# Kernel optimization log

Hardware: AMD Instinct MI355X
Metric: run time of the kernel (lower is better)

## Reference

```python
import jax, jax.numpy as jnp
import numpy as np

MODEL_DIM = 512
NUM_HEADS = 16
D_OUTPUT = 128
DIM_PER_HEAD = MODEL_DIM // NUM_HEADS  # 32
LN_EPS = 1e-5


def setup_inputs() -> dict:
    key = jax.random.key(0)
    ks = jax.random.split(key, 12)
    B = 128
    proj = MODEL_DIM * D_OUTPUT  # 65536
    s = 0.02
    return {
        "key": jax.random.normal(ks[0], (B, 1, MODEL_DIM), jnp.float32),
        "value": jax.random.normal(ks[1], (B, 1, MODEL_DIM), jnp.float32),
        "query": jax.random.normal(ks[2], (B, 1, MODEL_DIM), jnp.float32),
        "Wk": jax.random.normal(ks[3], (MODEL_DIM, proj), jnp.float32) * s,
        "bk": jnp.zeros((proj,), jnp.float32),
        "Wv": jax.random.normal(ks[4], (MODEL_DIM, proj), jnp.float32) * s,
        "bv": jnp.zeros((proj,), jnp.float32),
        "Wq": jax.random.normal(ks[5], (MODEL_DIM, proj), jnp.float32) * s,
        "bq": jnp.zeros((proj,), jnp.float32),
        "Wo": jax.random.normal(ks[6], (MODEL_DIM, MODEL_DIM), jnp.float32) * s,
        "bo": jnp.zeros((MODEL_DIM,), jnp.float32),
        "gamma": jnp.ones((MODEL_DIM,), jnp.float32),
        "beta": jnp.zeros((MODEL_DIM,), jnp.float32),
    }


def reference(key, value, query, Wk, bk, Wv, bv, Wq, bq, Wo, bo, gamma, beta):
    B = key.shape[0]
    residual = query  # [B, 1, model_dim]
    # QKV projections to model_dim*d_output, then view as (B*H, d_output, dim_per_head)
    k = (key @ Wk + bk).reshape(B * NUM_HEADS, -1, DIM_PER_HEAD)
    v = (value @ Wv + bv).reshape(B * NUM_HEADS, -1, DIM_PER_HEAD)
    q = (query @ Wq + bq).reshape(B * NUM_HEADS, -1, DIM_PER_HEAD)
    # faithful to original: scale = (dim_per_head // num_heads) ** -0.5 (int div)
    scale = (DIM_PER_HEAD // NUM_HEADS) ** (-0.5)
    scores = jnp.einsum('bqd,bkd->bqk', q, k) * scale  # [B*H, S, S]
    attn = jax.nn.softmax(scores, axis=2)
    context = jnp.einsum('bqk,bkd->bqd', attn, v)  # [B*H, S, dph]
    context = context.reshape(B, -1, DIM_PER_HEAD * NUM_HEADS)  # [B, d_output, model_dim]
    out = context @ Wo + bo
    x = residual + out  # broadcast [B,1,D] + [B,d_output,D]
    mu = jnp.mean(x, axis=-1, keepdims=True)
    var = jnp.mean(jnp.square(x - mu), axis=-1, keepdims=True)
    out = (x - mu) * jax.lax.rsqrt(var + LN_EPS) * gamma + beta
    return out, attn
```

## Files before the change

### kernel.cpp

```cpp
#include <hip/hip_runtime.h>

typedef unsigned short u16;
typedef unsigned int u32;
typedef __attribute__((ext_vector_type(4))) float f32x4;
typedef __attribute__((ext_vector_type(4))) u16 u16x4;
typedef __attribute__((ext_vector_type(8))) u16 u16x8;
typedef __attribute__((ext_vector_type(8))) __bf16 bf16x8;

#define DEV static __device__ __forceinline__

DEV u16 f2b(float f) {
  u32 u = __builtin_bit_cast(u32, f);
  u32 r = (u + 0x7fffu + ((u >> 16) & 1u)) >> 16;
  return (u16)r;
}

DEV bf16x8 mk8(u16x4 lo, u16x4 hi) {
  u16x8 v = __builtin_shufflevector(lo, hi, 0, 1, 2, 3, 4, 5, 6, 7);
  return __builtin_bit_cast(bf16x8, v);
}

__global__ __launch_bounds__(256) void prep_x(
    const float* __restrict__ key, const float* __restrict__ value,
    const float* __restrict__ query, u16* __restrict__ Xb)
{
  int idx = blockIdx.x * 256 + threadIdx.x;
  int mat = idx >> 14;
  int off = (idx & 16383) * 4;
  const float* src = mat == 0 ? key : (mat == 1 ? value : query);
  f32x4 v = *(const f32x4*)(src + off);
  u16x4 o;
#pragma unroll
  for (int i = 0; i < 4; ++i) o[i] = __builtin_bit_cast(u16, (__bf16)v[i]);
  *(u16x4*)(Xb + mat * 65536 + off) = o;
}

__global__ __launch_bounds__(256, 2) void qkv_gemm(
    const u16* __restrict__ Xb,
    const float* __restrict__ Wk, const float* __restrict__ bk,
    const float* __restrict__ Wv, const float* __restrict__ bv,
    const float* __restrict__ Wq, const float* __restrict__ bq,
    u16* __restrict__ Kp, u16* __restrict__ Vp, u16* __restrict__ Qp)
{
  const int mat = blockIdx.y;
  const float* W    = mat == 0 ? Wk : (mat == 1 ? Wv : Wq);
  const float* bias = mat == 0 ? bk : (mat == 1 ? bv : bq);
  u16* out          = mat == 0 ? Kp : (mat == 1 ? Vp : Qp);
  const u16* Xm = Xb + mat * 65536;
  const int n0 = blockIdx.x * 128;

  const int t = threadIdx.x, lane = t & 63, wid = t >> 6;
  const int wm = wid >> 1, wn = wid & 1;
  const int l15 = lane & 15, lg = lane >> 4;
  const int col0 = n0 + wn * 64 + l15;

  f32x4 acc[4][4];
#pragma unroll
  for (int i = 0; i < 4; ++i)
#pragma unroll
    for (int j = 0; j < 4; ++j) acc[i][j] = (f32x4){0.f, 0.f, 0.f, 0.f};

#pragma unroll 2
  for (int ks = 0; ks < 16; ++ks) {
    const int krow = ks * 32 + lg * 8;
    bf16x8 af[4];
#pragma unroll
    for (int mf = 0; mf < 4; ++mf)
      af[mf] = *(const bf16x8*)(Xm + (wm * 64 + mf * 16 + l15) * 512 + krow);
    float bb[8][4];
#pragma unroll
    for (int j = 0; j < 8; ++j) {
      const float* Wr = W + (size_t)(krow + j) * 65536 + col0;
#pragma unroll
      for (int nf = 0; nf < 4; ++nf) bb[j][nf] = Wr[nf * 16];
    }
    bf16x8 bfr[4];
#pragma unroll
    for (int nf = 0; nf < 4; ++nf) {
      bf16x8 v;
#pragma unroll
      for (int j = 0; j < 8; ++j) v[j] = (__bf16)bb[j][nf];
      bfr[nf] = v;
    }
#pragma unroll
    for (int mf = 0; mf < 4; ++mf)
#pragma unroll
      for (int nf = 0; nf < 4; ++nf)
        acc[mf][nf] = __builtin_amdgcn_mfma_f32_16x16x32_bf16(af[mf], bfr[nf], acc[mf][nf], 0, 0, 0);
  }

#pragma unroll
  for (int nf = 0; nf < 4; ++nf) {
    int col = wn * 64 + nf * 16 + l15;
    float bv_ = bias[n0 + col];
#pragma unroll
    for (int mf = 0; mf < 4; ++mf) {
      int row0 = wm * 64 + mf * 16 + lg * 4;
#pragma unroll
      for (int r = 0; r < 4; ++r) {
        out[(size_t)(row0 + r) * 65536 + n0 + col] = f2b(acc[mf][nf][r] + bv_);
      }
    }
  }
}

__global__ __launch_bounds__(256) void attn_kernel(
    const u16* __restrict__ Qp, const u16* __restrict__ Kp, const u16* __restrict__ Vp,
    float* __restrict__ attnOut, u16* __restrict__ ctx)
{
  const int bh = blockIdx.x;
  const int b = bh >> 4, h = bh & 15;
  const size_t base = (size_t)b * 65536 + h * 4096;

  __shared__ u16 qS[8 * 512];
  __shared__ u16 kS[8 * 512];
  __shared__ u16 vS[32 * 128];
  __shared__ u16 pS[32 * 512];

  const int t = threadIdx.x;
  const int lane = t & 63, w = t >> 6;
  const int l15 = lane & 15, lg = lane >> 4;

#pragma unroll
  for (int p = 0; p < 2; ++p) {
    int idx = p * 256 + t;
    int s = idx >> 2, dc = idx & 3;
    u16x8 qv = *(const u16x8*)(Qp + base + s * 32 + dc * 8);
    u16x8 kv = *(const u16x8*)(Kp + base + s * 32 + dc * 8);
    u16x8 vv = *(const u16x8*)(Vp + base + s * 32 + dc * 8);
    *(u16x4*)(qS + (dc * 2) * 512 + s * 4)     = __builtin_shufflevector(qv, qv, 0, 1, 2, 3);
    *(u16x4*)(qS + (dc * 2 + 1) * 512 + s * 4) = __builtin_shufflevector(qv, qv, 4, 5, 6, 7);
    *(u16x4*)(kS + (dc * 2) * 512 + s * 4)     = __builtin_shufflevector(kv, kv, 0, 1, 2, 3);
    *(u16x4*)(kS + (dc * 2 + 1) * 512 + s * 4) = __builtin_shufflevector(kv, kv, 4, 5, 6, 7);
#pragma unroll
    for (int i = 0; i < 8; ++i)
      vS[(s >> 2) * 128 + (dc * 8 + i) * 4 + (s & 3)] = vv[i];
  }
  __syncthreads();

  f32x4 sc[2][8];
#pragma unroll
  for (int i = 0; i < 2; ++i)
#pragma unroll
    for (int j = 0; j < 8; ++j) sc[i][j] = (f32x4){0.f, 0.f, 0.f, 0.f};

  {
    const int kqA = lg * 2;
    bf16x8 aq[2];
#pragma unroll
    for (int mf = 0; mf < 2; ++mf) {
      int m = w * 32 + mf * 16 + l15;
      u16x4 lo = *(const u16x4*)(qS + kqA * 512 + m * 4);
      u16x4 hi = *(const u16x4*)(qS + (kqA + 1) * 512 + m * 4);
      aq[mf] = mk8(lo, hi);
    }
#pragma unroll
    for (int nf = 0; nf < 8; ++nf) {
      int j = nf * 16 + l15;
      u16x4 lo = *(const u16x4*)(kS + kqA * 512 + j * 4);
      u16x4 hi = *(const u16x4*)(kS + (kqA + 1) * 512 + j * 4);
      bf16x8 bk8 = mk8(lo, hi);
#pragma unroll
      for (int mf = 0; mf < 2; ++mf)
        sc[mf][nf] = __builtin_amdgcn_mfma_f32_16x16x32_bf16(aq[mf], bk8, sc[mf][nf], 0, 0, 0);
    }
  }

  const float SCL = 0.70710678118654752f;
#pragma unroll
  for (int mf = 0; mf < 2; ++mf) {
#pragma unroll
    for (int r = 0; r < 4; ++r) {
      float m8 = -1e30f;
#pragma unroll
      for (int nf = 0; nf < 8; ++nf) m8 = fmaxf(m8, sc[mf][nf][r]);
      m8 = fmaxf(m8, __shfl_xor(m8, 1));
      m8 = fmaxf(m8, __shfl_xor(m8, 2));
      m8 = fmaxf(m8, __shfl_xor(m8, 4));
      m8 = fmaxf(m8, __shfl_xor(m8, 8));
      float s8 = 0.f;
#pragma unroll
      for (int nf = 0; nf < 8; ++nf) {
        float pv = __expf((sc[mf][nf][r] - m8) * SCL);
        sc[mf][nf][r] = pv;
        s8 += pv;
      }
      s8 += __shfl_xor(s8, 1);
      s8 += __shfl_xor(s8, 2);
      s8 += __shfl_xor(s8, 4);
      s8 += __shfl_xor(s8, 8);
      float inv = 1.0f / s8;
      int i = w * 32 + mf * 16 + lg * 4 + r;
      float* ao = attnOut + (size_t)bh * 16384 + (size_t)i * 128;
#pragma unroll
      for (int nf = 0; nf < 8; ++nf) {
        int j = nf * 16 + l15;
        float pv = sc[mf][nf][r] * inv;
        ao[j] = pv;
        pS[(j >> 2) * 512 + i * 4 + (j & 3)] = f2b(pv);
      }
    }
  }
  __syncthreads();

  f32x4 cacc[2][2];
#pragma unroll
  for (int i = 0; i < 2; ++i)
#pragma unroll
    for (int j = 0; j < 2; ++j) cacc[i][j] = (f32x4){0.f, 0.f, 0.f, 0.f};

#pragma unroll
  for (int ks2 = 0; ks2 < 4; ++ks2) {
    const int kqP = ks2 * 8 + lg * 2;
    bf16x8 ap[2];
#pragma unroll
    for (int mf = 0; mf < 2; ++mf) {
      int i = w * 32 + mf * 16 + l15;
      u16x4 lo = *(const u16x4*)(pS + kqP * 512 + i * 4);
      u16x4 hi = *(const u16x4*)(pS + (kqP + 1) * 512 + i * 4);
      ap[mf] = mk8(lo, hi);
    }
#pragma unroll
    for (int nf = 0; nf < 2; ++nf) {
      int d = nf * 16 + l15;
      u16x4 lo = *(const u16x4*)(vS + kqP * 128 + d * 4);
      u16x4 hi = *(const u16x4*)(vS + (kqP + 1) * 128 + d * 4);
      bf16x8 bv8 = mk8(lo, hi);
#pragma unroll
      for (int mf = 0; mf < 2; ++mf)
        cacc[mf][nf] = __builtin_amdgcn_mfma_f32_16x16x32_bf16(ap[mf], bv8, cacc[mf][nf], 0, 0, 0);
    }
  }

#pragma unroll
  for (int mf = 0; mf < 2; ++mf) {
#pragma unroll
    for (int r = 0; r < 4; ++r) {
      int s = w * 32 + mf * 16 + lg * 4 + r;
      size_t rowbase = ((size_t)b * 128 + h * 8 + (s >> 4)) * 512 + (s & 15) * 32;
#pragma unroll
      for (int nf = 0; nf < 2; ++nf) {
        int d = nf * 16 + l15;
        ctx[rowbase + d] = f2b(cacc[mf][nf][r]);
      }
    }
  }
}

__global__ __launch_bounds__(256) void out_proj(
    const u16* __restrict__ ctx, const float* __restrict__ Wo, const float* __restrict__ bo,
    const float* __restrict__ query, float* __restrict__ pre)
{
  const int m0 = blockIdx.x * 128;
  const int n0 = blockIdx.y * 128;

  __shared__ u16 As[16 * 512];
  __shared__ u16 Bs[16 * 512];

  const int t = threadIdx.x;
  const int lane = t & 63, wid = t >> 6;
  const int wm = wid >> 1, wn = wid & 1;
  const int l15 = lane & 15, lg = lane >> 4;

  f32x4 acc[4][4];
#pragma unroll
  for (int i = 0; i < 4; ++i)
#pragma unroll
    for (int j = 0; j < 4; ++j) acc[i][j] = (f32x4){0.f, 0.f, 0.f, 0.f};

  for (int it = 0; it < 8; ++it) {
    const int k0 = it * 64;
#pragma unroll
    for (int p = 0; p < 4; ++p) {
      int idx = p * 256 + t;
      int m = idx >> 3, dc = idx & 7;
      u16x8 av = *(const u16x8*)(ctx + (size_t)(m0 + m) * 512 + k0 + dc * 8);
      int kq = dc * 2;
      *(u16x4*)(As + kq * 512 + (((m + 2 * kq) & 127) << 2)) =
          __builtin_shufflevector(av, av, 0, 1, 2, 3);
      *(u16x4*)(As + (kq + 1) * 512 + (((m + 2 * (kq + 1)) & 127) << 2)) =
          __builtin_shufflevector(av, av, 4, 5, 6, 7);
    }
#pragma unroll
    for (int p = 0; p < 8; ++p) {
      int idx = p * 256 + t;
      int n = idx & 127, kq = idx >> 7;
      const float* wp = Wo + (size_t)(k0 + kq * 4) * 512 + n0 + n;
      u16x4 uv;
      uv[0] = f2b(wp[0]);
      uv[1] = f2b(wp[512]);
      uv[2] = f2b(wp[1024]);
      uv[3] = f2b(wp[1536]);
      *(u16x4*)(Bs + kq * 512 + n * 4) = uv;
    }
    __syncthreads();
#pragma unroll
    for (int kstep = 0; kstep < 2; ++kstep) {
      const int kqA = kstep * 8 + lg * 2;
      bf16x8 af[4], bfr[4];
#pragma unroll
      for (int mf = 0; mf < 4; ++mf) {
        int m = wm * 64 + mf * 16 + l15;
        u16x4 lo = *(const u16x4*)(As + kqA * 512 + (((m + 2 * kqA) & 127) << 2));
        u16x4 hi = *(const u16x4*)(As + (kqA + 1) * 512 + (((m + 2 * (kqA + 1)) & 127) << 2));
        af[mf] = mk8(lo, hi);
      }
#pragma unroll
      for (int nf = 0; nf < 4; ++nf) {
        int n = wn * 64 + nf * 16 + l15;
        u16x4 lo = *(const u16x4*)(Bs + kqA * 512 + n * 4);
        u16x4 hi = *(const u16x4*)(Bs + (kqA + 1) * 512 + n * 4);
        bfr[nf] = mk8(lo, hi);
      }
#pragma unroll
      for (int mf = 0; mf < 4; ++mf)
#pragma unroll
        for (int nf = 0; nf < 4; ++nf)
          acc[mf][nf] = __builtin_amdgcn_mfma_f32_16x16x32_bf16(af[mf], bfr[nf], acc[mf][nf], 0, 0, 0);
    }
    __syncthreads();
  }

#pragma unroll
  for (int nf = 0; nf < 4; ++nf) {
    int col = wn * 64 + nf * 16 + l15;
    float bv_ = bo[n0 + col];
#pragma unroll
    for (int mf = 0; mf < 4; ++mf) {
      int row0 = wm * 64 + mf * 16 + lg * 4;
#pragma unroll
      for (int r = 0; r < 4; ++r) {
        int m = m0 + row0 + r;
        float res = query[(m >> 7) * 512 + n0 + col];
        pre[(size_t)m * 512 + n0 + col] = acc[mf][nf][r] + bv_ + res;
      }
    }
  }
}

__global__ __launch_bounds__(256) void ln_kernel(
    const float* __restrict__ pre, const float* __restrict__ gamma,
    const float* __restrict__ beta, float* __restrict__ out0)
{
  const int w = threadIdx.x >> 6, lane = threadIdx.x & 63;
  const int row = blockIdx.x * 4 + w;
  const float* x = pre + (size_t)row * 512;
  f32x4 v0 = *(const f32x4*)(x + lane * 8);
  f32x4 v1 = *(const f32x4*)(x + lane * 8 + 4);
  float s = v0[0] + v0[1] + v0[2] + v0[3] + v1[0] + v1[1] + v1[2] + v1[3];
  float q = v0[0] * v0[0] + v0[1] * v0[1] + v0[2] * v0[2] + v0[3] * v0[3] +
            v1[0] * v1[0] + v1[1] * v1[1] + v1[2] * v1[2] + v1[3] * v1[3];
#pragma unroll
  for (int m = 1; m < 64; m <<= 1) {
    s += __shfl_xor(s, m);
    q += __shfl_xor(q, m);
  }
  float mean = s * (1.f / 512.f);
  float var = q * (1.f / 512.f) - mean * mean;
  float rs = rsqrtf(var + 1e-5f);
  f32x4 g0 = *(const f32x4*)(gamma + lane * 8);
  f32x4 g1 = *(const f32x4*)(gamma + lane * 8 + 4);
  f32x4 b0 = *(const f32x4*)(beta + lane * 8);
  f32x4 b1 = *(const f32x4*)(beta + lane * 8 + 4);
  f32x4 o0, o1;
#pragma unroll
  for (int i = 0; i < 4; ++i) {
    o0[i] = (v0[i] - mean) * rs * g0[i] + b0[i];
    o1[i] = (v1[i] - mean) * rs * g1[i] + b1[i];
  }
  *(f32x4*)(out0 + (size_t)row * 512 + lane * 8) = o0;
  *(f32x4*)(out0 + (size_t)row * 512 + lane * 8 + 4) = o1;
}

extern "C" void kernel_launch(void* const* d_in, const int* in_sizes, int n_in,
                              void* d_out, int out_size, void* d_ws, size_t ws_size,
                              hipStream_t stream) {
  (void)in_sizes; (void)n_in; (void)out_size; (void)ws_size;
  const float* key   = (const float*)d_in[0];
  const float* value = (const float*)d_in[1];
  const float* query = (const float*)d_in[2];
  const float* Wk    = (const float*)d_in[3];
  const float* bk    = (const float*)d_in[4];
  const float* Wv    = (const float*)d_in[5];
  const float* bv    = (const float*)d_in[6];
  const float* Wq    = (const float*)d_in[7];
  const float* bq    = (const float*)d_in[8];
  const float* Wo    = (const float*)d_in[9];
  const float* bo    = (const float*)d_in[10];
  const float* gamma = (const float*)d_in[11];
  const float* beta  = (const float*)d_in[12];

  char* ws = (char*)d_ws;
  u16* Kp  = (u16*)(ws + 0);
  u16* Vp  = (u16*)(ws + 16777216);
  u16* Qp  = (u16*)(ws + 33554432);
  u16* ctx = (u16*)(ws + 50331648);
  u16* Xb  = (u16*)(ws + 50331648);
  float* pre = (float*)(ws + 0);

  float* out0    = (float*)d_out;
  float* attnOut = out0 + 8388608;

  prep_x<<<dim3(192), 256, 0, stream>>>(key, value, query, Xb);
  qkv_gemm<<<dim3(512, 3), 256, 0, stream>>>(Xb, Wk, bk, Wv, bv, Wq, bq, Kp, Vp, Qp);
  attn_kernel<<<dim3(2048), 256, 0, stream>>>(Qp, Kp, Vp, attnOut, ctx);
  out_proj<<<dim3(128, 4), 256, 0, stream>>>(ctx, Wo, bo, query, pre);
  ln_kernel<<<dim3(4096), 256, 0, stream>>>(pre, gamma, beta, out0);
}
```

Before: 230.8 us.

## Stage QKV weights into LDS via async global_load_lds with double buffering

The QKV projection GEMM now copies fp32 weight tiles straight into shared memory with global_load_lds, using two buffers so the next 32-row K slice loads while the current one feeds MFMAs. The N tile per block doubles to 256 columns, halving the grid, and the shared-memory layout uses a rotating column skew to avoid bank conflicts on the transposed reads. This targets the cost of streaming 3x128MB of fp32 weights with scattered per-thread scalar loads. In exchange it uses 64KB of LDS per block, which may limit occupancy, and relies on hand-written waitcnt/barrier counts.

After: 198.6 us. 1.16x faster.

```diff
diff --git a/kernel.cpp b/kernel.cpp
--- a/kernel.cpp
+++ b/kernel.cpp
@@ -35,6 +35,49 @@
   *(u16x4*)(Xb + mat * 65536 + off) = o;
 }
 
+DEV void stage_w(const float* __restrict__ W, int K0, int n0,
+                 float* buf, int wv, int lane)
+{
+#pragma unroll
+  for (int p = 0; p < 8; ++p) {
+    int kl = wv * 8 + p;
+    int r = ((kl & 7) << 2) + (((kl >> 3) & 3) << 3);
+    int nphys = ((lane << 2) - r) & 255;
+    const float* gp = W + (size_t)(K0 + kl) * 65536 + n0 + nphys;
+    float* lp = buf + kl * 256;
+    __builtin_amdgcn_global_load_lds(
+        (const __attribute__((address_space(1))) u32*)gp,
+        (__attribute__((address_space(3))) u32*)lp, 16, 0, 0);
+  }
+}
+
+DEV void load_a(bf16x8* af, const u16* __restrict__ Xm, int kk,
+                int wm, int l15, int lg)
+{
+#pragma unroll
+  for (int mf = 0; mf < 4; ++mf)
+    af[mf] = *(const bf16x8*)(Xm + (wm * 64 + mf * 16 + l15) * 512 + kk + lg * 8);
+}
+
+DEV void compute_tile(const float* __restrict__ B, const bf16x8* af,
+                      f32x4 acc[4][8], int wn, int l15, int lg)
+{
+#pragma unroll
+  for (int nf = 0; nf < 8; ++nf) {
+    int bn0 = (wn * 128 + nf * 16 + l15 + 8 * lg) & 255;
+    float f[8];
+#pragma unroll
+    for (int j = 0; j < 8; ++j)
+      f[j] = B[(lg * 8 + j) * 256 + ((bn0 + 4 * j) & 255)];
+    bf16x8 bv;
+#pragma unroll
+    for (int j = 0; j < 8; ++j) bv[j] = (__bf16)f[j];
+#pragma unroll
+    for (int mf = 0; mf < 4; ++mf)
+      acc[mf][nf] = __builtin_amdgcn_mfma_f32_16x16x32_bf16(af[mf], bv, acc[mf][nf], 0, 0, 0);
+  }
+}
+
 __global__ __launch_bounds__(256, 2) void qkv_gemm(
     const u16* __restrict__ Xb,
     const float* __restrict__ Wk, const float* __restrict__ bk,
@@ -47,51 +90,45 @@
   const float* bias = mat == 0 ? bk : (mat == 1 ? bv : bq);
   u16* out          = mat == 0 ? Kp : (mat == 1 ? Vp : Qp);
   const u16* Xm = Xb + mat * 65536;
-  const int n0 = blockIdx.x * 128;
-
-  const int t = threadIdx.x, lane = t & 63, wid = t >> 6;
-  const int wm = wid >> 1, wn = wid & 1;
+  const int n0 = blockIdx.x * 256;
+
+  __shared__ float Bs0[32 * 256];
+  __shared__ float Bs1[32 * 256];
+
+  const int t = threadIdx.x, lane = t & 63, wv = t >> 6;
+  const int wm = wv >> 1, wn = wv & 1;
   const int l15 = lane & 15, lg = lane >> 4;
-  const int col0 = n0 + wn * 64 + l15;
-
-  f32x4 acc[4][4];
+
+  f32x4 acc[4][8];
 #pragma unroll
   for (int i = 0; i < 4; ++i)
 #pragma unroll
-    for (int j = 0; j < 4; ++j) acc[i][j] = (f32x4){0.f, 0.f, 0.f, 0.f};
-
-#pragma unroll 2
-  for (int ks = 0; ks < 16; ++ks) {
-    const int krow = ks * 32 + lg * 8;
-    bf16x8 af[4];
-#pragma unroll
-    for (int mf = 0; mf < 4; ++mf)
-      af[mf] = *(const bf16x8*)(Xm + (wm * 64 + mf * 16 + l15) * 512 + krow);
-    float bb[8][4];
-#pragma unroll
-    for (int j = 0; j < 8; ++j) {
-      const float* Wr = W + (size_t)(krow + j) * 65536 + col0;
-#pragma unroll
-      for (int nf = 0; nf < 4; ++nf) bb[j][nf] = Wr[nf * 16];
-    }
-    bf16x8 bfr[4];
-#pragma unroll
-    for (int nf = 0; nf < 4; ++nf) {
-      bf16x8 v;
-#pragma unroll
-      for (int j = 0; j < 8; ++j) v[j] = (__bf16)bb[j][nf];
-      bfr[nf] = v;
-    }
-#pragma unroll
-    for (int mf = 0; mf < 4; ++mf)
-#pragma unroll
-      for (int nf = 0; nf < 4; ++nf)
-        acc[mf][nf] = __builtin_amdgcn_mfma_f32_16x16x32_bf16(af[mf], bfr[nf], acc[mf][nf], 0, 0, 0);
-  }
-
-#pragma unroll
-  for (int nf = 0; nf < 4; ++nf) {
-    int col = wn * 64 + nf * 16 + l15;
+    for (int j = 0; j < 8; ++j) acc[i][j] = (f32x4){0.f, 0.f, 0.f, 0.f};
+
+  bf16x8 af0[4], af1[4];
+
+  stage_w(W, 0, n0, Bs0, wv, lane);
+  load_a(af0, Xm, 0, wm, l15, lg);
+
+  for (int it = 0; it < 16; it += 2) {
+    asm volatile("s_waitcnt vmcnt(4)" ::: "memory");
+    asm volatile("s_barrier" ::: "memory");
+    stage_w(W, (it + 1) * 32, n0, Bs1, wv, lane);
+    load_a(af1, Xm, (it + 1) * 32, wm, l15, lg);
+    compute_tile(Bs0, af0, acc, wn, l15, lg);
+
+    asm volatile("s_waitcnt vmcnt(4)" ::: "memory");
+    asm volatile("s_barrier" ::: "memory");
+    if (it + 2 < 16) {
+      stage_w(W, (it + 2) * 32, n0, Bs0, wv, lane);
+      load_a(af0, Xm, (it + 2) * 32, wm, l15, lg);
+    }
+    compute_tile(Bs1, af1, acc, wn, l15, lg);
+  }
+
+#pragma unroll
+  for (int nf = 0; nf < 8; ++nf) {
+    int col = wn * 128 + nf * 16 + l15;
     float bv_ = bias[n0 + col];
 #pragma unroll
     for (int mf = 0; mf < 4; ++mf) {
@@ -402,7 +439,7 @@
   float* attnOut = out0 + 8388608;
 
   prep_x<<<dim3(192), 256, 0, stream>>>(key, value, query, Xb);
-  qkv_gemm<<<dim3(512, 3), 256, 0, stream>>>(Xb, Wk, bk, Wv, bv, Wq, bq, Kp, Vp, Qp);
+  qkv_gemm<<<dim3(256, 3), 256, 0, stream>>>(Xb, Wk, bk, Wv, bv, Wq, bq, Kp, Vp, Qp);
   attn_kernel<<<dim3(2048), 256, 0, stream>>>(Qp, Kp, Vp, attnOut, ctx);
   out_proj<<<dim3(128, 4), 256, 0, stream>>>(ctx, Wo, bo, query, pre);
   ln_kernel<<<dim3(4096), 256, 0, stream>>>(pre, gamma, beta, out0);
```

## Stage QKV GEMM tiles through LDS with triple-buffered async global-to-LDS loads

Applied to the files above, without the earlier changes.

The QKV projection GEMM previously loaded fp32 weights and bf16 activations directly from global memory into registers each k-step, using strided scalar loads. It now copies 32x128 weight tiles and 128x32 activation tiles into LDS with global_load_lds, triple-buffered and issued two steps ahead, using a rotation swizzle to reduce bank conflicts. The grid is also flattened to 1D. The aim is to hide the latency of streaming the large weight matrices and to coalesce those loads, at the cost of about 72KB of LDS per block, which may cut occupancy, and of hand-tuned vmcnt waits.

Result: faster. 189.8 us (-17.8%).

```diff
diff --git a/kernel.cpp b/kernel.cpp
--- a/kernel.cpp
+++ b/kernel.cpp
@@ -35,6 +35,59 @@
   *(u16x4*)(Xb + mat * 65536 + off) = o;
 }
 
+DEV void stage_b(const float* __restrict__ W, int k0, int n0,
+                 float* buf, int wv, int lane)
+{
+#pragma unroll
+  for (int p = 0; p < 4; ++p) {
+    int q = wv * 4 + p;
+    int kl = q * 2 + (lane >> 5);
+    int rot = ((kl >> 3) & 1) << 4;
+    int nphys = (((lane & 31) << 2) - rot) & 127;
+    const float* gp = W + (size_t)(k0 + kl) * 65536 + n0 + nphys;
+    float* lp = buf + q * 256;
+    __builtin_amdgcn_global_load_lds(
+        (const __attribute__((address_space(1))) u32*)gp,
+        (__attribute__((address_space(3))) u32*)lp, 16, 0, 0);
+  }
+}
+
+DEV void stage_a(const u16* __restrict__ Xm, int k0,
+                 u16* buf, int wv, int lane)
+{
+#pragma unroll
+  for (int p = 0; p < 2; ++p) {
+    int q = wv * 2 + p;
+    int m = q * 16 + (lane >> 2);
+    const u16* gp = Xm + m * 512 + k0 + (lane & 3) * 8;
+    u16* lp = buf + q * 512;
+    __builtin_amdgcn_global_load_lds(
+        (const __attribute__((address_space(1))) u32*)gp,
+        (__attribute__((address_space(3))) u32*)lp, 16, 0, 0);
+  }
+}
+
+DEV void qkv_compute(const u16* __restrict__ A, const float* __restrict__ B,
+                     f32x4 acc[4][4], int wm, int wn, int l15, int lg)
+{
+  bf16x8 af[4];
+#pragma unroll
+  for (int mf = 0; mf < 4; ++mf)
+    af[mf] = *(const bf16x8*)(A + (wm * 64 + mf * 16 + l15) * 32 + lg * 8);
+  const int rot = (lg & 1) << 4;
+#pragma unroll
+  for (int nf = 0; nf < 4; ++nf) {
+    const int ncol = (wn * 64 + nf * 16 + l15 + rot) & 127;
+    bf16x8 bv;
+#pragma unroll
+    for (int j = 0; j < 8; ++j)
+      bv[j] = (__bf16)B[(lg * 8 + j) * 128 + ncol];
+#pragma unroll
+    for (int mf = 0; mf < 4; ++mf)
+      acc[mf][nf] = __builtin_amdgcn_mfma_f32_16x16x32_bf16(af[mf], bv, acc[mf][nf], 0, 0, 0);
+  }
+}
+
 __global__ __launch_bounds__(256, 2) void qkv_gemm(
     const u16* __restrict__ Xb,
     const float* __restrict__ Wk, const float* __restrict__ bk,
@@ -42,17 +95,20 @@
     const float* __restrict__ Wq, const float* __restrict__ bq,
     u16* __restrict__ Kp, u16* __restrict__ Vp, u16* __restrict__ Qp)
 {
-  const int mat = blockIdx.y;
+  const int bx = blockIdx.x;
+  const int mat = bx >> 9;
   const float* W    = mat == 0 ? Wk : (mat == 1 ? Wv : Wq);
   const float* bias = mat == 0 ? bk : (mat == 1 ? bv : bq);
   u16* out          = mat == 0 ? Kp : (mat == 1 ? Vp : Qp);
   const u16* Xm = Xb + mat * 65536;
-  const int n0 = blockIdx.x * 128;
-
-  const int t = threadIdx.x, lane = t & 63, wid = t >> 6;
-  const int wm = wid >> 1, wn = wid & 1;
+  const int n0 = (bx & 511) * 128;
+
+  __shared__ float Bs[3][32 * 128];
+  __shared__ u16   As[3][128 * 32];
+
+  const int t = threadIdx.x, lane = t & 63, wv = t >> 6;
+  const int wm = wv >> 1, wn = wv & 1;
   const int l15 = lane & 15, lg = lane >> 4;
-  const int col0 = n0 + wn * 64 + l15;
 
   f32x4 acc[4][4];
 #pragma unroll
@@ -60,34 +116,33 @@
 #pragma unroll
     for (int j = 0; j < 4; ++j) acc[i][j] = (f32x4){0.f, 0.f, 0.f, 0.f};
 
-#pragma unroll 2
-  for (int ks = 0; ks < 16; ++ks) {
-    const int krow = ks * 32 + lg * 8;
-    bf16x8 af[4];
-#pragma unroll
-    for (int mf = 0; mf < 4; ++mf)
-      af[mf] = *(const bf16x8*)(Xm + (wm * 64 + mf * 16 + l15) * 512 + krow);
-    float bb[8][4];
-#pragma unroll
-    for (int j = 0; j < 8; ++j) {
-      const float* Wr = W + (size_t)(krow + j) * 65536 + col0;
-#pragma unroll
-      for (int nf = 0; nf < 4; ++nf) bb[j][nf] = Wr[nf * 16];
-    }
-    bf16x8 bfr[4];
-#pragma unroll
-    for (int nf = 0; nf < 4; ++nf) {
-      bf16x8 v;
-#pragma unroll
-      for (int j = 0; j < 8; ++j) v[j] = (__bf16)bb[j][nf];
-      bfr[nf] = v;
-    }
-#pragma unroll
-    for (int mf = 0; mf < 4; ++mf)
-#pragma unroll
-      for (int nf = 0; nf < 4; ++nf)
-        acc[mf][nf] = __builtin_amdgcn_mfma_f32_16x16x32_bf16(af[mf], bfr[nf], acc[mf][nf], 0, 0, 0);
-  }
+  stage_b(W,  0, n0, &Bs[0][0], wv, lane);
+  stage_a(Xm, 0,     &As[0][0], wv, lane);
+  stage_b(W, 32, n0, &Bs[1][0], wv, lane);
+  stage_a(Xm, 32,    &As[1][0], wv, lane);
+
+#define QKV_ITER(T, WAITS, ISSUE)                                         \
+  {                                                                       \
+    asm volatile("s_waitcnt vmcnt(" WAITS ")" ::: "memory");              \
+    __builtin_amdgcn_sched_barrier(0);                                    \
+    __builtin_amdgcn_s_barrier();                                         \
+    __builtin_amdgcn_sched_barrier(0);                                    \
+    if (ISSUE) {                                                          \
+      stage_b(W,  ((T) + 2) * 32, n0, &Bs[((T) + 2) % 3][0], wv, lane);   \
+      stage_a(Xm, ((T) + 2) * 32,     &As[((T) + 2) % 3][0], wv, lane);   \
+    }                                                                     \
+    qkv_compute(&As[(T) % 3][0], &Bs[(T) % 3][0], acc, wm, wn, l15, lg);  \
+    __builtin_amdgcn_s_barrier();                                         \
+  }
+
+  QKV_ITER(0,  "6", 1)  QKV_ITER(1,  "6", 1)  QKV_ITER(2,  "6", 1)
+  QKV_ITER(3,  "6", 1)  QKV_ITER(4,  "6", 1)  QKV_ITER(5,  "6", 1)
+  QKV_ITER(6,  "6", 1)  QKV_ITER(7,  "6", 1)  QKV_ITER(8,  "6", 1)
+  QKV_ITER(9,  "6", 1)  QKV_ITER(10, "6", 1)  QKV_ITER(11, "6", 1)
+  QKV_ITER(12, "6", 1)  QKV_ITER(13, "6", 1)
+  QKV_ITER(14, "6", 0)
+  QKV_ITER(15, "0", 0)
+#undef QKV_ITER
 
 #pragma unroll
   for (int nf = 0; nf < 4; ++nf) {
@@ -402,7 +457,7 @@
   float* attnOut = out0 + 8388608;
 
   prep_x<<<dim3(192), 256, 0, stream>>>(key, value, query, Xb);
-  qkv_gemm<<<dim3(512, 3), 256, 0, stream>>>(Xb, Wk, bk, Wv, bv, Wq, bq, Kp, Vp, Qp);
+  qkv_gemm<<<dim3(1536), 256, 0, stream>>>(Xb, Wk, bk, Wv, bv, Wq, bq, Kp, Vp, Qp);
   attn_kernel<<<dim3(2048), 256, 0, stream>>>(Qp, Kp, Vp, attnOut, ctx);
   out_proj<<<dim3(128, 4), 256, 0, stream>>>(ctx, Wo, bo, query, pre);
   ln_kernel<<<dim3(4096), 256, 0, stream>>>(pre, gamma, beta, out0);
```

## Stage QKV GEMM tiles through double-buffered LDS and coalesce output stores

Applied to the files above, without the earlier changes.

The QKV projection GEMM now loads W tiles with coalesced 16-byte vector reads and X tiles via direct global-to-LDS loads into swizzled, double-buffered shared memory. Previously each lane issued strided scalar fp32 loads straight from global memory. Outputs of both the GEMM and the attention kernel are staged in LDS so the global stores are wide and coalesced. The grid is flattened and the occupancy hint raised, at the cost of extra LDS use and synchronisation.

After: 192.0 us. -16.8%, faster.

```diff
diff --git a/kernel.cpp b/kernel.cpp
--- a/kernel.cpp
+++ b/kernel.cpp
@@ -35,24 +35,30 @@
   *(u16x4*)(Xb + mat * 65536 + off) = o;
 }
 
-__global__ __launch_bounds__(256, 2) void qkv_gemm(
+__global__ __launch_bounds__(256, 3) void qkv_gemm(
     const u16* __restrict__ Xb,
     const float* __restrict__ Wk, const float* __restrict__ bk,
     const float* __restrict__ Wv, const float* __restrict__ bv,
     const float* __restrict__ Wq, const float* __restrict__ bq,
     u16* __restrict__ Kp, u16* __restrict__ Vp, u16* __restrict__ Qp)
 {
-  const int mat = blockIdx.y;
+  const int bx = blockIdx.x;
+  const int mat = bx >> 9;
   const float* W    = mat == 0 ? Wk : (mat == 1 ? Wv : Wq);
   const float* bias = mat == 0 ? bk : (mat == 1 ? bv : bq);
   u16* out          = mat == 0 ? Kp : (mat == 1 ? Vp : Qp);
   const u16* Xm = Xb + mat * 65536;
-  const int n0 = blockIdx.x * 128;
-
-  const int t = threadIdx.x, lane = t & 63, wid = t >> 6;
-  const int wm = wid >> 1, wn = wid & 1;
+  const int n0 = (bx & 511) * 128;
+
+  __shared__ float Bs[2][32 * 128];
+  __shared__ u16   As[2][128 * 32];
+
+  const int t0 = threadIdx.x, lane = t0 & 63, wv = t0 >> 6;
+  const int wm = wv >> 1, wn = wv & 1;
   const int l15 = lane & 15, lg = lane >> 4;
-  const int col0 = n0 + wn * 64 + l15;
+
+  const int brow = wv * 8 + (lane >> 5);
+  const int bcol = (lane & 31) * 4;
 
   f32x4 acc[4][4];
 #pragma unroll
@@ -60,35 +66,87 @@
 #pragma unroll
     for (int j = 0; j < 4; ++j) acc[i][j] = (f32x4){0.f, 0.f, 0.f, 0.f};
 
-#pragma unroll 2
-  for (int ks = 0; ks < 16; ++ks) {
-    const int krow = ks * 32 + lg * 8;
-    bf16x8 af[4];
-#pragma unroll
-    for (int mf = 0; mf < 4; ++mf)
-      af[mf] = *(const bf16x8*)(Xm + (wm * 64 + mf * 16 + l15) * 512 + krow);
-    float bb[8][4];
-#pragma unroll
-    for (int j = 0; j < 8; ++j) {
-      const float* Wr = W + (size_t)(krow + j) * 65536 + col0;
-#pragma unroll
-      for (int nf = 0; nf < 4; ++nf) bb[j][nf] = Wr[nf * 16];
-    }
-    bf16x8 bfr[4];
-#pragma unroll
-    for (int nf = 0; nf < 4; ++nf) {
-      bf16x8 v;
-#pragma unroll
-      for (int j = 0; j < 8; ++j) v[j] = (__bf16)bb[j][nf];
-      bfr[nf] = v;
-    }
-#pragma unroll
-    for (int mf = 0; mf < 4; ++mf)
-#pragma unroll
-      for (int nf = 0; nf < 4; ++nf)
-        acc[mf][nf] = __builtin_amdgcn_mfma_f32_16x16x32_bf16(af[mf], bfr[nf], acc[mf][nf], 0, 0, 0);
-  }
-
+  {
+    f32x4 rB[4];
+#pragma unroll
+    for (int p = 0; p < 4; ++p) {
+      int row = brow + p * 2;
+      rB[p] = *(const f32x4*)(W + (size_t)row * 65536 + n0 + bcol);
+    }
+#pragma unroll
+    for (int p = 0; p < 2; ++p) {
+      int q = wv * 2 + p;
+      int m = q * 16 + (lane >> 2);
+      int sc = ((lane & 3) - ((m >> 1) & 3)) & 3;
+      const u16* gp = Xm + m * 512 + sc * 8;
+      u16* lp = &As[0][q * 512];
+      __builtin_amdgcn_global_load_lds(
+          (const __attribute__((address_space(1))) u32*)gp,
+          (__attribute__((address_space(3))) u32*)lp, 16, 0, 0);
+    }
+#pragma unroll
+    for (int p = 0; p < 4; ++p) {
+      int row = brow + p * 2;
+      int pc = (bcol + (((row >> 3) & 1) << 4)) & 127;
+      *(f32x4*)&Bs[0][row * 128 + pc] = rB[p];
+    }
+    __syncthreads();
+  }
+
+  for (int t = 0; t < 16; ++t) {
+    const int cur = t & 1, nxt = cur ^ 1;
+    f32x4 rB[4];
+    if (t < 15) {
+      const int k0n = (t + 1) * 32;
+#pragma unroll
+      for (int p = 0; p < 4; ++p) {
+        int row = brow + p * 2;
+        rB[p] = *(const f32x4*)(W + (size_t)(k0n + row) * 65536 + n0 + bcol);
+      }
+#pragma unroll
+      for (int p = 0; p < 2; ++p) {
+        int q = wv * 2 + p;
+        int m = q * 16 + (lane >> 2);
+        int sc = ((lane & 3) - ((m >> 1) & 3)) & 3;
+        const u16* gp = Xm + m * 512 + k0n + sc * 8;
+        u16* lp = &As[nxt][q * 512];
+        __builtin_amdgcn_global_load_lds(
+            (const __attribute__((address_space(1))) u32*)gp,
+            (__attribute__((address_space(3))) u32*)lp, 16, 0, 0);
+      }
+    }
+    __builtin_amdgcn_sched_barrier(0);
+    {
+      bf16x8 af[4];
+#pragma unroll
+      for (int mf = 0; mf < 4; ++mf) {
+        int m = wm * 64 + mf * 16 + l15;
+        af[mf] = *(const bf16x8*)&As[cur][m * 32 + ((lg + ((m >> 1) & 3)) & 3) * 8];
+      }
+#pragma unroll
+      for (int nf = 0; nf < 4; ++nf) {
+        int pc = (wn * 64 + nf * 16 + l15 + ((lg & 1) << 4)) & 127;
+        bf16x8 bv;
+#pragma unroll
+        for (int j = 0; j < 8; ++j) bv[j] = (__bf16)Bs[cur][(lg * 8 + j) * 128 + pc];
+#pragma unroll
+        for (int mf = 0; mf < 4; ++mf)
+          acc[mf][nf] = __builtin_amdgcn_mfma_f32_16x16x32_bf16(af[mf], bv, acc[mf][nf], 0, 0, 0);
+      }
+    }
+    __builtin_amdgcn_sched_barrier(0);
+    if (t < 15) {
+#pragma unroll
+      for (int p = 0; p < 4; ++p) {
+        int row = brow + p * 2;
+        int pc = (bcol + (((row >> 3) & 1) << 4)) & 127;
+        *(f32x4*)&Bs[nxt][row * 128 + pc] = rB[p];
+      }
+    }
+    __syncthreads();
+  }
+
+  u16* tile = (u16*)&Bs[0][0];
 #pragma unroll
   for (int nf = 0; nf < 4; ++nf) {
     int col = wn * 64 + nf * 16 + l15;
@@ -97,10 +155,17 @@
     for (int mf = 0; mf < 4; ++mf) {
       int row0 = wm * 64 + mf * 16 + lg * 4;
 #pragma unroll
-      for (int r = 0; r < 4; ++r) {
-        out[(size_t)(row0 + r) * 65536 + n0 + col] = f2b(acc[mf][nf][r] + bv_);
-      }
-    }
+      for (int r = 0; r < 4; ++r)
+        tile[(row0 + r) * 128 + col] = f2b(acc[mf][nf][r] + bv_);
+    }
+  }
+  __syncthreads();
+#pragma unroll
+  for (int rr = 0; rr < 16; ++rr) {
+    int row = wv * 32 + rr * 2 + (lane >> 5);
+    int c = (lane & 31) * 4;
+    u16x4 v = *(const u16x4*)&tile[row * 128 + c];
+    *(u16x4*)(out + (size_t)row * 65536 + n0 + c) = v;
   }
 }
 
@@ -232,18 +297,25 @@
     }
   }
 
+  __syncthreads();
 #pragma unroll
   for (int mf = 0; mf < 2; ++mf) {
 #pragma unroll
     for (int r = 0; r < 4; ++r) {
       int s = w * 32 + mf * 16 + lg * 4 + r;
-      size_t rowbase = ((size_t)b * 128 + h * 8 + (s >> 4)) * 512 + (s & 15) * 32;
+      int p = s >> 4, q = s & 15;
 #pragma unroll
       for (int nf = 0; nf < 2; ++nf) {
         int d = nf * 16 + l15;
-        ctx[rowbase + d] = f2b(cacc[mf][nf][r]);
-      }
-    }
+        pS[p * 512 + q * 32 + d] = f2b(cacc[mf][nf][r]);
+      }
+    }
+  }
+#pragma unroll
+  for (int pp = 0; pp < 2; ++pp) {
+    int p = w * 2 + pp;
+    u16x8 v = *(const u16x8*)&pS[p * 512 + lane * 8];
+    *(u16x8*)(ctx + ((size_t)b * 128 + h * 8 + p) * 512 + lane * 8) = v;
   }
 }
 
@@ -402,7 +474,7 @@
   float* attnOut = out0 + 8388608;
 
   prep_x<<<dim3(192), 256, 0, stream>>>(key, value, query, Xb);
-  qkv_gemm<<<dim3(512, 3), 256, 0, stream>>>(Xb, Wk, bk, Wv, bv, Wq, bq, Kp, Vp, Qp);
+  qkv_gemm<<<dim3(1536), 256, 0, stream>>>(Xb, Wk, bk, Wv, bv, Wq, bq, Kp, Vp, Qp);
   attn_kernel<<<dim3(2048), 256, 0, stream>>>(Qp, Kp, Vp, attnOut, ctx);
   out_proj<<<dim3(128, 4), 256, 0, stream>>>(ctx, Wo, bo, query, pre);
   ln_kernel<<<dim3(4096), 256, 0, stream>>>(pre, gamma, beta, out0);
```
